# Kernel tuning notes

Hardware: AMD Instinct MI355X
Metric: run time of the kernel (lower is better)

Reference implementation:

```python
import jax, jax.numpy as jnp
import numpy as np

S = 7
B = 2
C = 80
N = 8192
LAMBD_COORD = 5.0
LAMBD_NOOBJ = 0.5


def setup_inputs() -> dict:
    key = jax.random.key(0)
    k1, k2, k3 = jax.random.split(key, 3)
    prediction = jax.random.uniform(k1, (N, S, S, B * 5 + C), dtype=jnp.float32)
    target = jax.random.uniform(k2, (N, S, S, 5 + C), dtype=jnp.float32)
    conf = (jax.random.uniform(k3, (N, S, S)) > 0.7).astype(jnp.float32)
    target = target.at[..., 4].set(conf)
    return {"prediction": prediction, "target": target}


def _rel2abs(box):
    # box: (N,S,S,>=4) with (xcr_rcell, ycr_rcell, wr, hr); returns corner coords (image-relative)
    x, y, w, h = box[..., 0], box[..., 1], box[..., 2], box[..., 3]
    jj = jnp.arange(S, dtype=box.dtype)[None, None, :]   # cell_j -> x axis
    ii = jnp.arange(S, dtype=box.dtype)[None, :, None]   # cell_i -> y axis
    xc = (x + jj) / S
    yc = (y + ii) / S
    return xc - w / 2, yc - h / 2, xc + w / 2, yc + h / 2


def _iou(a, b):
    ax1, ay1, ax2, ay2 = a
    bx1, by1, bx2, by2 = b
    iw = jnp.clip(jnp.minimum(ax2, bx2) - jnp.maximum(ax1, bx1), 0.0)
    ih = jnp.clip(jnp.minimum(ay2, by2) - jnp.maximum(ay1, by1), 0.0)
    inter = iw * ih
    area_a = (ax2 - ax1) * (ay2 - ay1)
    area_b = (bx2 - bx1) * (by2 - by1)
    return inter / (area_a + area_b - inter + 1e-6)


def reference(prediction, target):
    tgt_abs = _rel2abs(target[..., :5])
    iou0 = _iou(tgt_abs, _rel2abs(prediction[..., 0:5]))
    iou1 = _iou(tgt_abs, _rel2abs(prediction[..., 5:10]))
    # faithful to source: mask True (iou0 > iou1) selects offset idx = 5 (second box)
    sel_mask = (iou0 > iou1)[..., None]                              # (N,S,S,1)
    box_sel = jnp.where(sel_mask, prediction[..., 5:10], prediction[..., 0:5])
    xy_hat = box_sel[..., 0:2]
    wh_hat = box_sel[..., 2:4]

    xy = target[..., 0:2]
    wh = target[..., 2:4]
    # faithful to source: pred_c uses box_k after the loop, i.e. 4 + 5*(B-1)
    pred_c = prediction[..., 4 + 5 * (B - 1)]
    true_c = target[..., 4]

    obj = (true_c != 0)                  # contributions kept where object present
    objf = obj.astype(prediction.dtype)
    noobjf = 1.0 - objf

    # xy loss
    loss_xy_cell = objf * jnp.sum((xy - xy_hat) ** 2, axis=-1)

    # wh loss with sqrt-safe masking (masked entries contribute 0, matching masked_fill)
    obj_e = obj[..., None]
    wh_safe = jnp.where(obj_e, wh, 1.0)
    wh_hat_safe = jnp.where(obj_e, jnp.maximum(wh_hat, 0.0), 1.0)
    loss_wh_cell = objf * jnp.sum((jnp.sqrt(wh_safe) - jnp.sqrt(wh_hat_safe)) ** 2, axis=-1)

    # confidence losses
    conf_se = (true_c - pred_c) ** 2
    loss_conf_obj_cell = objf * conf_se
    loss_conf_noobj_cell = noobjf * conf_se

    # class loss
    pred_class = prediction[..., 5 * B:]
    true_class = target[..., 5:]
    loss_class_cell = objf * jnp.sum((true_class - pred_class) ** 2, axis=-1)

    bs = prediction.shape[0]
    loss_xy = jnp.sum(loss_xy_cell) / bs
    loss_wh = jnp.sum(loss_wh_cell) / bs
    loss_conf_obj = jnp.sum(loss_conf_obj_cell) / bs
    loss_conf_noobj = jnp.sum(loss_conf_noobj_cell) / bs
    loss_class = jnp.sum(loss_class_cell) / bs

    # faithful to source: weighted sum divided by BATCH_SIZE once more
    loss = (LAMBD_COORD * loss_xy + LAMBD_COORD * loss_wh + loss_conf_obj
            + LAMBD_NOOBJ * loss_conf_noobj + loss_class) / bs
    return loss, loss_xy, loss_wh, loss_conf_obj, loss_conf_noobj, loss_class
```

## Files before the change

### kernel.cpp

```cpp
#include <hip/hip_runtime.h>


#define NCELLS (8192 * 49)
#define TILE_CELLS 32
#define NTILES (NCELLS / TILE_CELLS)
#define TPB 8
#define NBLOCKS (NTILES / TPB)
#define T_FLOATS (TILE_CELLS * 85)
#define P_FLOATS (TILE_CELLS * 90)
#define BUF_FLOATS (T_FLOATS + P_FLOATS)
#define T_CHUNKS (T_FLOATS / 4)
#define TOT_CHUNKS (BUF_FLOATS / 4)
#define W_CHUNKS (TOT_CHUNKS / 4)

constexpr float BSF = 8192.0f;

__device__ __forceinline__ void g2lds16(const float* g, float* s) {
    __builtin_amdgcn_global_load_lds(
        (const __attribute__((address_space(1))) void*)g,
        (__attribute__((address_space(3))) void*)s,
        16, 0, 0);
}

__device__ __forceinline__ void rel2abs(float x, float y, float w, float h,
                                        float fi, float fj,
                                        float& x1, float& y1, float& x2, float& y2) {
    float xc = (x + fj) / 7.0f;
    float yc = (y + fi) / 7.0f;
    float hw = w * 0.5f, hh = h * 0.5f;
    x1 = xc - hw; y1 = yc - hh; x2 = xc + hw; y2 = yc + hh;
}

__device__ __forceinline__ float iou_abs(float ax1, float ay1, float ax2, float ay2,
                                         float bx1, float by1, float bx2, float by2) {
    float iw = fminf(ax2, bx2) - fmaxf(ax1, bx1); iw = fmaxf(iw, 0.0f);
    float ih = fminf(ay2, by2) - fmaxf(ay1, by1); ih = fmaxf(ih, 0.0f);
    float inter  = iw * ih;
    float area_a = (ax2 - ax1) * (ay2 - ay1);
    float area_b = (bx2 - bx1) * (by2 - by1);
    return inter / (area_a + area_b - inter + 1e-6f);
}

__device__ __forceinline__ void stage_tile(const float* __restrict__ pred,
                                           const float* __restrict__ tgt,
                                           float* lbuf, int tile,
                                           int wid, int lane) {
    const float* tg = tgt  + (size_t)tile * T_FLOATS;
    const float* pg = pred + (size_t)tile * P_FLOATS;
    #pragma unroll
    for (int i = 0; i < 5; ++i) {
        const int q = W_CHUNKS * wid + 64 * i + lane;
        const float* src = (q < T_CHUNKS) ? (tg + 4 * q) : (pg + 4 * (q - T_CHUNKS));
        g2lds16(src, lbuf + 4 * q);
    }
    {
        const int cw = 320 + lane;
        if (cw < W_CHUNKS) {
            const int q = W_CHUNKS * wid + cw;
            const float* src = (q < T_CHUNKS) ? (tg + 4 * q) : (pg + 4 * (q - T_CHUNKS));
            g2lds16(src, lbuf + 4 * q);
        }
    }
}

__global__ __launch_bounds__(256) void yolo_main(const float* __restrict__ pred,
                                                 const float* __restrict__ tgt,
                                                 float* __restrict__ acc,
                                                 int nrep, int sstride) {
    __shared__ __align__(16) float lds[2][BUF_FLOATS];
    __shared__ float smr[4 * 5];

    const int tid  = threadIdx.x;
    const int lane = tid & 63;
    const int wid  = tid >> 6;

    float a_xy = 0.f, a_wh = 0.f, a_co = 0.f, a_cn = 0.f, a_cl = 0.f;

    const int tile0 = blockIdx.x * TPB;

    stage_tile(pred, tgt, &lds[0][0], tile0, wid, lane);

    for (int it = 0; it < TPB; ++it) {
        if (it + 1 < TPB) {
            stage_tile(pred, tgt, &lds[(it + 1) & 1][0], tile0 + it + 1, wid, lane);
            asm volatile("s_waitcnt vmcnt(6)" ::: "memory");
        } else {
            asm volatile("s_waitcnt vmcnt(0)" ::: "memory");
        }
        __builtin_amdgcn_s_barrier();
        asm volatile("" ::: "memory");

        {
            const float* buf  = &lds[it & 1][0];
            const int   cell  = lane & 31;
            const int   half  = lane >> 5;
            const float* tb   = buf + 85 * cell;
            const float* pb   = buf + T_FLOATS + 90 * cell;

            const float objf = (tb[4] != 0.0f) ? 1.0f : 0.0f;

            const int c0 = 20 * wid + 10 * half;
            float s = 0.f;
            #pragma unroll
            for (int k = 0; k < 10; ++k) {
                float d = tb[5 + c0 + k] - pb[10 + c0 + k];
                s = fmaf(d, d, s);
            }
            a_cl += objf * s;

            if (half == 0 && wid == (it & 3)) {
                float tx = tb[0], ty = tb[1], tw = tb[2], th = tb[3], tc = tb[4];
                float p0x = pb[0], p0y = pb[1], p0w = pb[2], p0h = pb[3];
                float p1x = pb[5], p1y = pb[6], p1w = pb[7], p1h = pb[8];
                float pc  = pb[9];

                int gcell = (tile0 + it) * TILE_CELLS + cell;
                int sij   = gcell % 49;
                float fi  = (float)(sij / 7);
                float fj  = (float)(sij % 7);

                float t1, t2, t3, t4, a1, a2, a3, a4, b1, b2, b3, b4;
                rel2abs(tx,  ty,  tw,  th,  fi, fj, t1, t2, t3, t4);
                rel2abs(p0x, p0y, p0w, p0h, fi, fj, a1, a2, a3, a4);
                rel2abs(p1x, p1y, p1w, p1h, fi, fj, b1, b2, b3, b4);

                float iou0 = iou_abs(t1, t2, t3, t4, a1, a2, a3, a4);
                float iou1 = iou_abs(t1, t2, t3, t4, b1, b2, b3, b4);

                bool sel = iou0 > iou1;
                float xh = sel ? p1x : p0x;
                float yh = sel ? p1y : p0y;
                float wh = sel ? p1w : p0w;
                float hh = sel ? p1h : p0h;

                float obx = (tc != 0.0f) ? 1.0f : 0.0f;

                float dx = tx - xh, dy = ty - yh;
                a_xy += obx * (dx * dx + dy * dy);

                float sw = sqrtf(tw) - sqrtf(fmaxf(wh, 0.0f));
                float sh = sqrtf(th) - sqrtf(fmaxf(hh, 0.0f));
                a_wh += obx * (sw * sw + sh * sh);

                float ce = tc - pc; ce *= ce;
                a_co += obx * ce;
                a_cn += (1.0f - obx) * ce;
            }
        }

        asm volatile("" ::: "memory");
        __builtin_amdgcn_s_barrier();
    }

    #pragma unroll
    for (int off = 32; off; off >>= 1) {
        a_xy += __shfl_down(a_xy, off, 64);
        a_wh += __shfl_down(a_wh, off, 64);
        a_co += __shfl_down(a_co, off, 64);
        a_cn += __shfl_down(a_cn, off, 64);
        a_cl += __shfl_down(a_cl, off, 64);
    }
    if (lane == 0) {
        smr[wid * 5 + 0] = a_xy; smr[wid * 5 + 1] = a_wh; smr[wid * 5 + 2] = a_co;
        smr[wid * 5 + 3] = a_cn; smr[wid * 5 + 4] = a_cl;
    }
    __syncthreads();
    if (tid == 0) {
        float s0 = 0.f, s1 = 0.f, s2 = 0.f, s3 = 0.f, s4 = 0.f;
        #pragma unroll
        for (int w = 0; w < 4; ++w) {
            s0 += smr[w * 5 + 0]; s1 += smr[w * 5 + 1]; s2 += smr[w * 5 + 2];
            s3 += smr[w * 5 + 3]; s4 += smr[w * 5 + 4];
        }
        const int rep = (int)(blockIdx.x & (unsigned)(nrep - 1));
        float* a0 = acc + (size_t)rep * 5 * sstride;
        atomicAdd(&a0[0 * sstride], s0);
        atomicAdd(&a0[1 * sstride], s1);
        atomicAdd(&a0[2 * sstride], s2);
        atomicAdd(&a0[3 * sstride], s3);
        atomicAdd(&a0[4 * sstride], s4);
    }
}

__global__ void yolo_finalize(const float* __restrict__ acc, float* __restrict__ out,
                              int nrep, int sstride) {
    if (threadIdx.x == 0 && blockIdx.x == 0) {
        float s[5] = {0.f, 0.f, 0.f, 0.f, 0.f};
        for (int r = 0; r < nrep; ++r)
            for (int k = 0; k < 5; ++k)
                s[k] += acc[((size_t)r * 5 + k) * sstride];
        float lxy = s[0] / BSF;
        float lwh = s[1] / BSF;
        float lco = s[2] / BSF;
        float lcn = s[3] / BSF;
        float lcl = s[4] / BSF;
        out[0] = (5.0f * lxy + 5.0f * lwh + lco + 0.5f * lcn + lcl) / BSF;
        out[1] = lxy;
        out[2] = lwh;
        out[3] = lco;
        out[4] = lcn;
        out[5] = lcl;
    }
}

extern "C" void kernel_launch(void* const* d_in, const int* in_sizes, int n_in,
                              void* d_out, int out_size, void* d_ws, size_t ws_size,
                              hipStream_t stream) {
    const float* pred = (const float*)d_in[0];
    const float* tgt  = (const float*)d_in[1];
    float* out = (float*)d_out;
    float* acc = (float*)d_ws;

    int nrep, sstride; size_t zbytes;
    if (ws_size >= 8 * 5 * 32 * sizeof(float)) { nrep = 8; sstride = 32; zbytes = 8 * 5 * 32 * sizeof(float); }
    else                                       { nrep = 1; sstride = 1;  zbytes = 5 * sizeof(float); }

    hipMemsetAsync(acc, 0, zbytes, stream);

    yolo_main<<<NBLOCKS, 256, 0, stream>>>(pred, tgt, acc, nrep, sstride);
    yolo_finalize<<<1, 64, 0, stream>>>(acc, out, nrep, sstride);
}
```

Before: 309.7 us.

## Give each wave private double-buffered LDS tiles and drop block barriers

Replaces the block-shared 32-cell tile pipeline with per-wave 8-cell tiles, each wave staging and consuming its own double buffer. This removes the two s_barrier calls per iteration and the cross-wave dependency. It also changes the work mapping to 8 lanes per cell with the box/IoU work on one lane per cell, rather than one wave per iteration. In exchange, many more blocks are launched, each wave handles only 4 tiles, and the per-wave pipeline is short, so prologue latency is exposed more often.

```diff
diff --git a/kernel.cpp b/kernel.cpp
--- a/kernel.cpp
+++ b/kernel.cpp
@@ -2,16 +2,14 @@
 
 
 #define NCELLS (8192 * 49)
-#define TILE_CELLS 32
-#define NTILES (NCELLS / TILE_CELLS)
-#define TPB 8
-#define NBLOCKS (NTILES / TPB)
-#define T_FLOATS (TILE_CELLS * 85)
-#define P_FLOATS (TILE_CELLS * 90)
-#define BUF_FLOATS (T_FLOATS + P_FLOATS)
-#define T_CHUNKS (T_FLOATS / 4)
-#define TOT_CHUNKS (BUF_FLOATS / 4)
-#define W_CHUNKS (TOT_CHUNKS / 4)
+#define CPT 8
+#define TPW 4
+#define WPB 4
+#define CELLS_PER_BLOCK (CPT * TPW * WPB)
+#define NBLOCKS (NCELLS / CELLS_PER_BLOCK)
+#define TFL (CPT * 85)
+#define PFL (CPT * 90)
+#define BUF_FL (TFL + PFL)
 
 constexpr float BSF = 8192.0f;
 
@@ -41,115 +39,107 @@
     return inter / (area_a + area_b - inter + 1e-6f);
 }
 
-__device__ __forceinline__ void stage_tile(const float* __restrict__ pred,
-                                           const float* __restrict__ tgt,
-                                           float* lbuf, int tile,
-                                           int wid, int lane) {
-    const float* tg = tgt  + (size_t)tile * T_FLOATS;
-    const float* pg = pred + (size_t)tile * P_FLOATS;
-    #pragma unroll
-    for (int i = 0; i < 5; ++i) {
-        const int q = W_CHUNKS * wid + 64 * i + lane;
-        const float* src = (q < T_CHUNKS) ? (tg + 4 * q) : (pg + 4 * (q - T_CHUNKS));
-        g2lds16(src, lbuf + 4 * q);
-    }
-    {
-        const int cw = 320 + lane;
-        if (cw < W_CHUNKS) {
-            const int q = W_CHUNKS * wid + cw;
-            const float* src = (q < T_CHUNKS) ? (tg + 4 * q) : (pg + 4 * (q - T_CHUNKS));
-            g2lds16(src, lbuf + 4 * q);
-        }
-    }
+__device__ __forceinline__ void stage_tile(const float* __restrict__ tg,
+                                           const float* __restrict__ pg,
+                                           float* wbuf, int lane) {
+    g2lds16(tg + 4 * lane,         wbuf + 4 * lane);
+    g2lds16(tg + 4 * (64 + lane),  wbuf + 4 * (64 + lane));
+    if (lane < 42)
+        g2lds16(tg + 4 * (128 + lane), wbuf + 4 * (128 + lane));
+    g2lds16(pg + 4 * lane,         wbuf + TFL + 4 * lane);
+    g2lds16(pg + 4 * (64 + lane),  wbuf + TFL + 4 * (64 + lane));
+    if (lane < 52)
+        g2lds16(pg + 4 * (128 + lane), wbuf + TFL + 4 * (128 + lane));
 }
 
 __global__ __launch_bounds__(256) void yolo_main(const float* __restrict__ pred,
                                                  const float* __restrict__ tgt,
                                                  float* __restrict__ acc,
                                                  int nrep, int sstride) {
-    __shared__ __align__(16) float lds[2][BUF_FLOATS];
-    __shared__ float smr[4 * 5];
+    __shared__ __align__(16) float lds[WPB][2][BUF_FL];
+    __shared__ float smr[WPB * 5];
 
     const int tid  = threadIdx.x;
     const int lane = tid & 63;
     const int wid  = tid >> 6;
 
+    float* const wb0 = &lds[wid][0][0];
+    float* const wb1 = &lds[wid][1][0];
+
+    const int wave_id = blockIdx.x * WPB + wid;
+    const int tile0   = wave_id * TPW;
+
     float a_xy = 0.f, a_wh = 0.f, a_co = 0.f, a_cn = 0.f, a_cl = 0.f;
 
-    const int tile0 = blockIdx.x * TPB;
-
-    stage_tile(pred, tgt, &lds[0][0], tile0, wid, lane);
-
-    for (int it = 0; it < TPB; ++it) {
-        if (it + 1 < TPB) {
-            stage_tile(pred, tgt, &lds[(it + 1) & 1][0], tile0 + it + 1, wid, lane);
+    const int cell = lane >> 3;
+    const int part = lane & 7;
+    const int c0   = 10 * part;
+
+    stage_tile(tgt + (size_t)tile0 * TFL, pred + (size_t)tile0 * PFL, wb0, lane);
+
+    #pragma unroll
+    for (int k = 0; k < TPW; ++k) {
+        float* const cur = (k & 1) ? wb1 : wb0;
+        float* const nxt = (k & 1) ? wb0 : wb1;
+
+        if (k + 1 < TPW) {
+            asm volatile("s_waitcnt lgkmcnt(0)" ::: "memory");
+            const int t = tile0 + k + 1;
+            stage_tile(tgt + (size_t)t * TFL, pred + (size_t)t * PFL, nxt, lane);
             asm volatile("s_waitcnt vmcnt(6)" ::: "memory");
         } else {
             asm volatile("s_waitcnt vmcnt(0)" ::: "memory");
         }
-        __builtin_amdgcn_s_barrier();
-        asm volatile("" ::: "memory");
-
-        {
-            const float* buf  = &lds[it & 1][0];
-            const int   cell  = lane & 31;
-            const int   half  = lane >> 5;
-            const float* tb   = buf + 85 * cell;
-            const float* pb   = buf + T_FLOATS + 90 * cell;
-
-            const float objf = (tb[4] != 0.0f) ? 1.0f : 0.0f;
-
-            const int c0 = 20 * wid + 10 * half;
-            float s = 0.f;
-            #pragma unroll
-            for (int k = 0; k < 10; ++k) {
-                float d = tb[5 + c0 + k] - pb[10 + c0 + k];
-                s = fmaf(d, d, s);
-            }
-            a_cl += objf * s;
-
-            if (half == 0 && wid == (it & 3)) {
-                float tx = tb[0], ty = tb[1], tw = tb[2], th = tb[3], tc = tb[4];
-                float p0x = pb[0], p0y = pb[1], p0w = pb[2], p0h = pb[3];
-                float p1x = pb[5], p1y = pb[6], p1w = pb[7], p1h = pb[8];
-                float pc  = pb[9];
-
-                int gcell = (tile0 + it) * TILE_CELLS + cell;
-                int sij   = gcell % 49;
-                float fi  = (float)(sij / 7);
-                float fj  = (float)(sij % 7);
-
-                float t1, t2, t3, t4, a1, a2, a3, a4, b1, b2, b3, b4;
-                rel2abs(tx,  ty,  tw,  th,  fi, fj, t1, t2, t3, t4);
-                rel2abs(p0x, p0y, p0w, p0h, fi, fj, a1, a2, a3, a4);
-                rel2abs(p1x, p1y, p1w, p1h, fi, fj, b1, b2, b3, b4);
-
-                float iou0 = iou_abs(t1, t2, t3, t4, a1, a2, a3, a4);
-                float iou1 = iou_abs(t1, t2, t3, t4, b1, b2, b3, b4);
-
-                bool sel = iou0 > iou1;
-                float xh = sel ? p1x : p0x;
-                float yh = sel ? p1y : p0y;
-                float wh = sel ? p1w : p0w;
-                float hh = sel ? p1h : p0h;
-
-                float obx = (tc != 0.0f) ? 1.0f : 0.0f;
-
-                float dx = tx - xh, dy = ty - yh;
-                a_xy += obx * (dx * dx + dy * dy);
-
-                float sw = sqrtf(tw) - sqrtf(fmaxf(wh, 0.0f));
-                float sh = sqrtf(th) - sqrtf(fmaxf(hh, 0.0f));
-                a_wh += obx * (sw * sw + sh * sh);
-
-                float ce = tc - pc; ce *= ce;
-                a_co += obx * ce;
-                a_cn += (1.0f - obx) * ce;
-            }
-        }
-
-        asm volatile("" ::: "memory");
-        __builtin_amdgcn_s_barrier();
+
+        const float* tb = cur + 85 * cell;
+        const float* pb = cur + TFL + 90 * cell;
+
+        const float objf = (tb[4] != 0.0f) ? 1.0f : 0.0f;
+
+        float s = 0.f;
+        #pragma unroll
+        for (int c = 0; c < 10; ++c) {
+            float d = tb[5 + c0 + c] - pb[10 + c0 + c];
+            s = fmaf(d, d, s);
+        }
+        a_cl += objf * s;
+
+        if (part == 0) {
+            float tx = tb[0], ty = tb[1], tw = tb[2], th = tb[3], tc = tb[4];
+            float p0x = pb[0], p0y = pb[1], p0w = pb[2], p0h = pb[3];
+            float p1x = pb[5], p1y = pb[6], p1w = pb[7], p1h = pb[8];
+            float pc  = pb[9];
+
+            int gcell = (tile0 + k) * CPT + cell;
+            int sij   = gcell % 49;
+            float fi  = (float)(sij / 7);
+            float fj  = (float)(sij % 7);
+
+            float t1, t2, t3, t4, a1, a2, a3, a4, b1, b2, b3, b4;
+            rel2abs(tx,  ty,  tw,  th,  fi, fj, t1, t2, t3, t4);
+            rel2abs(p0x, p0y, p0w, p0h, fi, fj, a1, a2, a3, a4);
+            rel2abs(p1x, p1y, p1w, p1h, fi, fj, b1, b2, b3, b4);
+
+            float iou0 = iou_abs(t1, t2, t3, t4, a1, a2, a3, a4);
+            float iou1 = iou_abs(t1, t2, t3, t4, b1, b2, b3, b4);
+
+            bool sel = iou0 > iou1;
+            float xh = sel ? p1x : p0x;
+            float yh = sel ? p1y : p0y;
+            float wh = sel ? p1w : p0w;
+            float hh = sel ? p1h : p0h;
+
+            float dx = tx - xh, dy = ty - yh;
+            a_xy += objf * (dx * dx + dy * dy);
+
+            float sw = sqrtf(tw) - sqrtf(fmaxf(wh, 0.0f));
+            float sh = sqrtf(th) - sqrtf(fmaxf(hh, 0.0f));
+            a_wh += objf * (sw * sw + sh * sh);
+
+            float ce = tc - pc; ce *= ce;
+            a_co += objf * ce;
+            a_cn += (1.0f - objf) * ce;
+        }
     }
 
     #pragma unroll
```

New measurement: 300.5 us. 3.0% less time.
